# Kernel optimization log

Hardware: AMD Instinct MI355X
Metric: run time of the kernel (lower is better)

The kernel has to match this reference:

```python
import jax, jax.numpy as jnp
import numpy as np

NUM_HEADS = 16
QMAX = 127.0  # int8 symmetric

def fake_quant(x):
    # symmetric per-tensor int8 quantize -> dequantize (models Quantize/QLinear numerics)
    scale = jnp.maximum(jnp.max(jnp.abs(x)) / QMAX, 1e-8)
    q = jnp.clip(jnp.round(x / scale), -QMAX, QMAX) * scale
    # straight-through estimator (no-op in fwd-only, keeps fwd/bwd code identical)
    return x + jax.lax.stop_gradient(q - x)

def setup_inputs() -> dict:
    key = jax.random.key(0)
    ks = jax.random.split(key, 5)
    B, T, C = 2, 2048, 1024
    return {
        "x": jax.random.normal(ks[0], (B, T, C), jnp.float32),
        "Wqkv": jax.random.normal(ks[1], (3 * C, C), jnp.float32) * (C ** -0.5),
        "bqkv": jax.random.normal(ks[2], (3 * C,), jnp.float32) * 0.01,
        "Wproj": jax.random.normal(ks[3], (C, C), jnp.float32) * (C ** -0.5),
        "bproj": jax.random.normal(ks[4], (C,), jnp.float32) * 0.01,
    }

def reference(x, Wqkv, bqkv, Wproj, bproj):
    B, T, C = x.shape
    H = NUM_HEADS
    D = C // H
    scale = D ** -0.5
    # quantized input + quantized-weight linear (dequantized to fp32 afterwards)
    xq = fake_quant(x)
    qkv = xq @ fake_quant(Wqkv).T + bqkv                      # [B, T, 3C]
    qkv = qkv.reshape(B, T, 3, H, D).transpose(2, 0, 3, 1, 4)  # [3, B, H, T, D]
    q, k, v = qkv[0], qkv[1], qkv[2]
    scores = jnp.einsum("bhqd,bhkd->bhqk", q, k) * scale       # [B, H, T, T]
    causal = jnp.triu(jnp.full((T, T), -jnp.inf, jnp.float32), k=1)
    attn = jax.nn.softmax(scores + causal, axis=-1)
    # dropout: eval mode -> identity
    out = jnp.einsum("bhqk,bhkd->bhqd", attn, v)               # [B, H, T, D]
    out = out.transpose(0, 2, 1, 3).reshape(B, T, C)
    outq = fake_quant(out)
    return outq @ fake_quant(Wproj).T + bproj
```

## Files before the change

kernel.cpp:

```cpp
#include <hip/hip_runtime.h>
#include <hip/hip_bf16.h>
#include <stdint.h>

typedef __bf16 bf16_t;
typedef bf16_t bf16x4 __attribute__((ext_vector_type(4)));
typedef bf16_t bf16x8 __attribute__((ext_vector_type(8)));
typedef short s16x4 __attribute__((ext_vector_type(4)));
typedef int i32x4 __attribute__((ext_vector_type(4)));
typedef float f32x4 __attribute__((ext_vector_type(4)));
typedef unsigned int u32;
typedef u32 u32x4 __attribute__((ext_vector_type(4)));
typedef u32 u32x2 __attribute__((ext_vector_type(2)));

#define QMAXF 127.0f
#define CSC 0.18033688f

__device__ __forceinline__ void gl16(const void* g, void* l) {
  __builtin_amdgcn_global_load_lds(
      (__attribute__((address_space(1))) void*)(g),
      (__attribute__((address_space(3))) void*)(l), 16, 0, 0);
}

__global__ __launch_bounds__(256) void amax3_kernel(const float* __restrict__ p0, int n0,
                                                    const float* __restrict__ p1, int n1,
                                                    const float* __restrict__ p2, int n2,
                                                    float* __restrict__ dst) {
  const float* p; int n; float* d; int b0, nb;
  if (blockIdx.x < 512)      { p = p0; n = n0; d = dst + 0; b0 = 0;   nb = 512; }
  else if (blockIdx.x < 768) { p = p1; n = n1; d = dst + 1; b0 = 512; nb = 256; }
  else                       { p = p2; n = n2; d = dst + 2; b0 = 768; nb = 128; }
  const int n4 = n >> 2;
  const int stride = nb * 256;
  float m = 0.f;
  for (int i = (blockIdx.x - b0) * 256 + threadIdx.x; i < n4; i += stride) {
    const f32x4 v = ((const f32x4*)p)[i];
    m = fmaxf(m, fmaxf(fmaxf(fabsf(v[0]), fabsf(v[1])), fmaxf(fabsf(v[2]), fabsf(v[3]))));
  }
#pragma unroll
  for (int dd = 1; dd < 64; dd <<= 1) m = fmaxf(m, __shfl_xor(m, dd));
  __shared__ float sm[4];
  if ((threadIdx.x & 63) == 0) sm[threadIdx.x >> 6] = m;
  __syncthreads();
  if (threadIdx.x == 0) {
    float mm = fmaxf(fmaxf(sm[0], sm[1]), fmaxf(sm[2], sm[3]));
    atomicMax((int*)d, __float_as_int(mm));
  }
}

__device__ __forceinline__ void quant_body(const float* __restrict__ p, int n,
                                           const float* __restrict__ amax,
                                           int8_t* __restrict__ q, int bid, int nb) {
  const float s = fmaxf(amax[0] / QMAXF, 1e-8f);
  const int n4 = n >> 2;
  const int stride = nb * 256;
  for (int i = bid * 256 + (int)threadIdx.x; i < n4; i += stride) {
    const f32x4 v = ((const f32x4*)p)[i];
    int r[4];
#pragma unroll
    for (int j = 0; j < 4; j++) {
      float t = rintf(v[j] / s);
      t = fminf(127.f, fmaxf(-127.f, t));
      r[j] = (int)t;
    }
    ((uint32_t*)q)[i] = (uint32_t)(r[0] & 0xff) | ((uint32_t)(r[1] & 0xff) << 8) |
                        ((uint32_t)(r[2] & 0xff) << 16) | ((uint32_t)(r[3] & 0xff) << 24);
  }
}

__global__ __launch_bounds__(256) void quant3_kernel(const float* __restrict__ p0, int n0,
                                                     const float* __restrict__ p1, int n1,
                                                     const float* __restrict__ p2, int n2,
                                                     const float* __restrict__ amax,
                                                     int8_t* __restrict__ q0,
                                                     int8_t* __restrict__ q1,
                                                     int8_t* __restrict__ q2) {
  if (blockIdx.x < 512)      quant_body(p0, n0, amax + 0, q0, blockIdx.x, 512);
  else if (blockIdx.x < 768) quant_body(p1, n1, amax + 1, q1, blockIdx.x - 512, 256);
  else                       quant_body(p2, n2, amax + 2, q2, blockIdx.x - 768, 128);
}

__global__ __launch_bounds__(256) void quant_bf16_kernel(const u32* __restrict__ p,
                                                         int n,
                                                         const float* __restrict__ amax,
                                                         int8_t* __restrict__ q) {
  const float s = fmaxf(amax[0] / QMAXF, 1e-8f);
  const int n8 = n >> 3;
  const int stride = gridDim.x * blockDim.x;
  for (int i = blockIdx.x * blockDim.x + (int)threadIdx.x; i < n8; i += stride) {
    const u32x4 v = ((const u32x4*)p)[i];
    int r[8];
#pragma unroll
    for (int k = 0; k < 4; k++) {
      const float lo = __uint_as_float(v[k] << 16);
      const float hi = __uint_as_float(v[k] & 0xffff0000u);
      float t0 = fminf(127.f, fmaxf(-127.f, rintf(lo / s)));
      float t1 = fminf(127.f, fmaxf(-127.f, rintf(hi / s)));
      r[2 * k] = (int)t0; r[2 * k + 1] = (int)t1;
    }
    u32x2 o;
    o[0] = (u32)(r[0] & 0xff) | ((u32)(r[1] & 0xff) << 8) |
           ((u32)(r[2] & 0xff) << 16) | ((u32)(r[3] & 0xff) << 24);
    o[1] = (u32)(r[4] & 0xff) | ((u32)(r[5] & 0xff) << 8) |
           ((u32)(r[6] & 0xff) << 16) | ((u32)(r[7] & 0xff) << 24);
    ((u32x2*)q)[i] = o;
  }
}

template <int MODE>
__global__ __launch_bounds__(256) void gemm_i8_kernel(
    const int8_t* __restrict__ A, const int8_t* __restrict__ Bw,
    const float* __restrict__ amaxA, const float* __restrict__ amaxB,
    const float* __restrict__ bias,
    bf16_t* __restrict__ qkv_out, bf16_t* __restrict__ vt_out, float* __restrict__ f_out) {
  constexpr int K = 1024;
  __shared__ int8_t As[2][8192];
  __shared__ int8_t Bs[2][8192];
  const int tid = threadIdx.x;
  const int lane = tid & 63;
  const int w = tid >> 6, wr = w >> 1, wc = w & 1;
  const int l15 = lane & 15, lg = lane >> 4;
  const int bm = blockIdx.y * 128, bn = blockIdx.x * 128;

  const int sr = tid >> 2;
  const int sc = (tid & 3) * 16;
  const int8_t* gA = A + (size_t)(bm + sr) * K + sc;
  const int8_t* gB = Bw + (size_t)(bn + sr) * K + sc;

  auto stage = [&](int k0, int buf) {
    gl16(gA + k0, As[buf] + tid * 16);
    gl16(gA + 64 * K + k0, As[buf] + 4096 + tid * 16);
    gl16(gB + k0, Bs[buf] + tid * 16);
    gl16(gB + 64 * K + k0, Bs[buf] + 4096 + tid * 16);
  };

  i32x4 acc[4][4] = {};

  stage(0, 0);
  __syncthreads();
  for (int ks = 0; ks < K / 64; ks++) {
    const int buf = ks & 1;
    if (ks + 1 < K / 64) stage((ks + 1) * 64, buf ^ 1);
    i32x4 aF[4], bF[4];
#pragma unroll
    for (int m = 0; m < 4; m++)
      aF[m] = *(const i32x4*)(As[buf] + (wr * 64 + m * 16 + l15) * 64 + lg * 16);
#pragma unroll
    for (int n = 0; n < 4; n++)
      bF[n] = *(const i32x4*)(Bs[buf] + (wc * 64 + n * 16 + l15) * 64 + lg * 16);
#pragma unroll
    for (int m = 0; m < 4; m++)
#pragma unroll
      for (int n = 0; n < 4; n++)
        acc[m][n] = __builtin_amdgcn_mfma_i32_16x16x64_i8(aF[m], bF[n], acc[m][n], 0, 0, 0);
    __syncthreads();
  }

  const float sA = fmaxf(amaxA[0] / QMAXF, 1e-8f);
  const float sB = fmaxf(amaxB[0] / QMAXF, 1e-8f);
  const float s = sA * sB;

#pragma unroll
  for (int m = 0; m < 4; m++) {
#pragma unroll
    for (int n = 0; n < 4; n++) {
      const int c = bn + wc * 64 + n * 16 + l15;
      const float bs = bias[c];
      const int r0 = bm + wr * 64 + m * 16 + lg * 4;
      float vv[4];
#pragma unroll
      for (int reg = 0; reg < 4; reg++) vv[reg] = (float)acc[m][n][reg] * s + bs;
      if (MODE == 0) {
        const int which = c >> 10, hd = c & 1023;
        if (which < 2) {
          const float qs = (which == 0) ? CSC : 1.0f;
#pragma unroll
          for (int reg = 0; reg < 4; reg++) {
            const int r = r0 + reg;
            const int b = r >> 11, t = r & 2047;
            qkv_out[(size_t)which * (32u * 2048 * 64) +
                    (size_t)((((b << 4) + (hd >> 6)) * 2048 + t) << 6) + (hd & 63)] =
                (bf16_t)(vv[reg] * qs);
          }
        } else {
          const int b = r0 >> 11, t0 = r0 & 2047;
          const int h = hd >> 6, d = hd & 63;
          bf16x4 pk;
#pragma unroll
          for (int reg = 0; reg < 4; reg++) pk[reg] = (bf16_t)vv[reg];
          *(bf16x4*)(vt_out + ((size_t)((b << 4) + h) * 64 + d) * 2048 + t0) = pk;
        }
      } else {
#pragma unroll
        for (int reg = 0; reg < 4; reg++) f_out[(size_t)(r0 + reg) * 1024 + c] = vv[reg];
      }
    }
  }
}

__global__ __launch_bounds__(256, 2) void attn_kernel(
    const bf16_t* __restrict__ Qg, const bf16_t* __restrict__ Kg, const bf16_t* __restrict__ VTg,
    bf16_t* __restrict__ Out, float* __restrict__ amax_out) {
  const int bh = blockIdx.x;
  const int pairi = blockIdx.y;
  const int tid = threadIdx.x, lane = tid & 63, w = tid >> 6;
  const int l15 = lane & 15, lg = lane >> 4;
  const int b = bh >> 4, h = bh & 15;

  const bf16_t* Qp = Qg + (size_t)bh * 2048 * 64;
  const char* Kbase = (const char*)(Kg + (size_t)bh * 2048 * 64);
  const char* Vbase = (const char*)(VTg + (size_t)bh * 64 * 2048);

  __shared__ __align__(16) bf16_t Kb[3][4096];
  __shared__ __align__(16) bf16_t Vb[3][4096];

  auto stage = [&](int kv0, int buf) {
#pragma unroll
    for (int i = 0; i < 4; i++) {
      const int o = ((w & 1) * 4 + i) * 1024 + lane * 16;
      const int row = o >> 7;
      const int sbc = (o & 127) ^ ((row & 7) << 4);
      if (w < 2)
        gl16(Kbase + (size_t)(kv0 + row) * 128 + sbc, (char*)Kb[buf] + o);
      else
        gl16(Vbase + (size_t)row * 4096 + (size_t)kv0 * 2 + sbc, (char*)Vb[buf] + o);
    }
  };

  float am = 0.f;
  for (int half = 0; half < 2; ++half) {
    const int S = half ? (31 - pairi) : pairi;
    const int qb = S * 64 + w * 16;
    const int nt = S + 1;
    const int qrow = qb + l15;

    bf16x8 qf[2];
#pragma unroll
    for (int ks = 0; ks < 2; ks++)
      qf[ks] = *(const bf16x8*)(Qp + (size_t)(qb + l15) * 64 + ks * 32 + lg * 8);

    f32x4 acc[4] = {};
    float lsum = 0.f;

    stage(0, 0);
    if (nt > 1) stage(64, 1);

    for (int it = 0; it < nt; ++it) {
      const int sl = it % 3;
      const int kv0 = it * 64;

      if (it + 1 < nt) { asm volatile("s_waitcnt vmcnt(4)" ::: "memory"); }
      else             { asm volatile("s_waitcnt vmcnt(0)" ::: "memory"); }
      __builtin_amdgcn_sched_barrier(0);
      __builtin_amdgcn_s_barrier();
      __builtin_amdgcn_sched_barrier(0);

      if (it + 2 < nt) stage(kv0 + 128, (it + 2) % 3);

      bf16x8 kF[4][2];
#pragma unroll
      for (int rf = 0; rf < 4; rf++)
#pragma unroll
        for (int ks = 0; ks < 2; ks++) {
          const int row = rf * 16 + l15;
          kF[rf][ks] = *(const bf16x8*)((const char*)Kb[sl] + row * 128 +
                                        ((ks * 64 + lg * 16) ^ ((row & 7) << 4)));
        }
      s16x4 vB[4][4];
#pragma unroll
      for (int cf = 0; cf < 4; cf++)
#pragma unroll
        for (int rf = 0; rf < 4; rf++) {
          const int row = cf * 16 + l15;
          vB[cf][rf] = *(const s16x4*)((const char*)Vb[sl] + row * 128 +
                                       ((rf * 32 + lg * 8) ^ ((row & 7) << 4)));
        }

      f32x4 sfT[4] = {};
      __builtin_amdgcn_s_setprio(1);
#pragma unroll
      for (int rf = 0; rf < 4; rf++)
#pragma unroll
        for (int ks = 0; ks < 2; ks++)
          sfT[rf] = __builtin_amdgcn_mfma_f32_16x16x32_bf16(kF[rf][ks], qf[ks], sfT[rf], 0, 0, 0);
      __builtin_amdgcn_s_setprio(0);

      const bool need_mask = (it == nt - 1);
      float p[16];
#pragma unroll
      for (int rf = 0; rf < 4; rf++)
#pragma unroll
        for (int reg = 0; reg < 4; reg++) {
          float v = sfT[rf][reg];
          if (need_mask && (kv0 + rf * 16 + lg * 4 + reg > qrow)) v = -1e30f;
          p[rf * 4 + reg] = __builtin_amdgcn_exp2f(v);
        }
      float s01 = (p[0] + p[1]) + (p[2] + p[3]);
      float s23 = (p[4] + p[5]) + (p[6] + p[7]);
      float s45 = (p[8] + p[9]) + (p[10] + p[11]);
      float s67 = (p[12] + p[13]) + (p[14] + p[15]);
      lsum += (s01 + s23) + (s45 + s67);

      s16x4 pa[4];
#pragma unroll
      for (int rf = 0; rf < 4; rf++) {
        bf16x4 t;
#pragma unroll
        for (int reg = 0; reg < 4; reg++) t[reg] = (bf16_t)p[rf * 4 + reg];
        pa[rf] = __builtin_bit_cast(s16x4, t);
      }
      __builtin_amdgcn_s_setprio(1);
#pragma unroll
      for (int cf = 0; cf < 4; cf++)
#pragma unroll
        for (int rf = 0; rf < 4; rf++)
          acc[cf] = __builtin_amdgcn_mfma_f32_16x16x16bf16_1k(pa[rf], vB[cf][rf], acc[cf], 0, 0, 0);
      __builtin_amdgcn_s_setprio(0);
    }

    lsum += __shfl_xor(lsum, 16);
    lsum += __shfl_xor(lsum, 32);
    const float inv = 1.0f / lsum;
    float iq[4];
#pragma unroll
    for (int reg = 0; reg < 4; reg++) iq[reg] = __shfl(inv, lg * 4 + reg);
#pragma unroll
    for (int cf = 0; cf < 4; cf++)
#pragma unroll
      for (int reg = 0; reg < 4; reg++) {
        const float v = acc[cf][reg] * iq[reg];
        am = fmaxf(am, fabsf(v));
        const int t = qb + lg * 4 + reg;
        Out[(size_t)(b * 2048 + t) * 1024 + h * 64 + cf * 16 + l15] = (bf16_t)v;
      }

    __syncthreads();
  }

#pragma unroll
  for (int dd = 1; dd < 64; dd <<= 1) am = fmaxf(am, __shfl_xor(am, dd));
  if (lane == 0) atomicMax((int*)amax_out, __float_as_int(am));
}

extern "C" void kernel_launch(void* const* d_in, const int* in_sizes, int n_in,
                              void* d_out, int out_size, void* d_ws, size_t ws_size,
                              hipStream_t stream) {
  const float* x = (const float*)d_in[0];
  const float* Wqkv = (const float*)d_in[1];
  const float* bqkv = (const float*)d_in[2];
  const float* Wproj = (const float*)d_in[3];
  const float* bproj = (const float*)d_in[4];
  float* out = (float*)d_out;

  char* ws = (char*)d_ws;
  float* amax = (float*)ws;
  int8_t* xq = (int8_t*)(ws + 256);
  int8_t* wqq = xq + (size_t)4096 * 1024;
  int8_t* wpq = wqq + (size_t)3072 * 1024;
  bf16_t* qkv = (bf16_t*)(ws + 8388864);
  bf16_t* Q = qkv;
  bf16_t* Kk = qkv + (size_t)32 * 2048 * 64;
  bf16_t* VT = qkv + (size_t)2 * 32 * 2048 * 64;
  bf16_t* aout = (bf16_t*)(ws + 33554688);
  int8_t* outq = (int8_t*)(ws + 50331904);

  hipMemsetAsync(amax, 0, 16, stream);
  amax3_kernel<<<896, 256, 0, stream>>>(x, 4194304, Wqkv, 3145728, Wproj, 1048576, amax);
  quant3_kernel<<<896, 256, 0, stream>>>(x, 4194304, Wqkv, 3145728, Wproj, 1048576, amax,
                                         xq, wqq, wpq);
  gemm_i8_kernel<0><<<dim3(24, 32), 256, 0, stream>>>(xq, wqq, amax + 0, amax + 1, bqkv,
                                                      qkv, VT, nullptr);
  attn_kernel<<<dim3(32, 16), 256, 0, stream>>>(Q, Kk, VT, aout, amax + 3);
  quant_bf16_kernel<<<512, 256, 0, stream>>>((const u32*)aout, 4194304, amax + 3, outq);
  gemm_i8_kernel<1><<<dim3(8, 32), 256, 0, stream>>>(outq, wpq, amax + 3, amax + 2, bproj,
                                                     nullptr, nullptr, out);
}
```

Measured before the change: 129.7 us.

## Restructure attention into single-wave blocks loading K/V directly from global

```diff
diff --git a/kernel.cpp b/kernel.cpp
--- a/kernel.cpp
+++ b/kernel.cpp
@@ -197,144 +197,106 @@
   }
 }
 
-__global__ __launch_bounds__(256, 2) void attn_kernel(
+__global__ __launch_bounds__(64, 3) void attn_kernel(
     const bf16_t* __restrict__ Qg, const bf16_t* __restrict__ Kg, const bf16_t* __restrict__ VTg,
     bf16_t* __restrict__ Out, float* __restrict__ amax_out) {
   const int bh = blockIdx.x;
-  const int pairi = blockIdx.y;
-  const int tid = threadIdx.x, lane = tid & 63, w = tid >> 6;
+  const int S = 127 - (int)blockIdx.y;
+  const int lane = threadIdx.x;
   const int l15 = lane & 15, lg = lane >> 4;
   const int b = bh >> 4, h = bh & 15;
 
   const bf16_t* Qp = Qg + (size_t)bh * 2048 * 64;
-  const char* Kbase = (const char*)(Kg + (size_t)bh * 2048 * 64);
-  const char* Vbase = (const char*)(VTg + (size_t)bh * 64 * 2048);
-
-  __shared__ __align__(16) bf16_t Kb[3][4096];
-  __shared__ __align__(16) bf16_t Vb[3][4096];
-
-  auto stage = [&](int kv0, int buf) {
-#pragma unroll
-    for (int i = 0; i < 4; i++) {
-      const int o = ((w & 1) * 4 + i) * 1024 + lane * 16;
-      const int row = o >> 7;
-      const int sbc = (o & 127) ^ ((row & 7) << 4);
-      if (w < 2)
-        gl16(Kbase + (size_t)(kv0 + row) * 128 + sbc, (char*)Kb[buf] + o);
-      else
-        gl16(Vbase + (size_t)row * 4096 + (size_t)kv0 * 2 + sbc, (char*)Vb[buf] + o);
-    }
-  };
-
+  const bf16_t* Kp = Kg + (size_t)bh * 2048 * 64;
+  const bf16_t* Vp = VTg + (size_t)bh * 64 * 2048;
+
+  const int qb = S * 16;
+  const int nt = (S >> 2) + 1;
+  const int qrow = qb + l15;
+
+  bf16x8 qf[2];
+#pragma unroll
+  for (int ks = 0; ks < 2; ks++)
+    qf[ks] = *(const bf16x8*)(Qp + (size_t)(qb + l15) * 64 + ks * 32 + lg * 8);
+
+  f32x4 acc[4] = {};
+  float lsum = 0.f;
+
+  for (int it = 0; it < nt; ++it) {
+    const int kv0 = it * 64;
+
+    bf16x8 kF[4][2];
+#pragma unroll
+    for (int rf = 0; rf < 4; rf++)
+#pragma unroll
+      for (int ks = 0; ks < 2; ks++)
+        kF[rf][ks] = *(const bf16x8*)(Kp + (size_t)(kv0 + rf * 16 + l15) * 64 + ks * 32 + lg * 8);
+
+    s16x4 vB[4][4];
+#pragma unroll
+    for (int cf = 0; cf < 4; cf++)
+#pragma unroll
+      for (int rf = 0; rf < 4; rf++)
+        vB[cf][rf] = *(const s16x4*)(Vp + (size_t)(cf * 16 + l15) * 2048 + kv0 + rf * 16 + lg * 4);
+
+    f32x4 sfT[4] = {};
+    __builtin_amdgcn_s_setprio(1);
+#pragma unroll
+    for (int rf = 0; rf < 4; rf++)
+#pragma unroll
+      for (int ks = 0; ks < 2; ks++)
+        sfT[rf] = __builtin_amdgcn_mfma_f32_16x16x32_bf16(kF[rf][ks], qf[ks], sfT[rf], 0, 0, 0);
+    __builtin_amdgcn_s_setprio(0);
+
+    const bool need_mask = (it == nt - 1);
+    float p[16];
+#pragma unroll
+    for (int rf = 0; rf < 4; rf++)
+#pragma unroll
+      for (int reg = 0; reg < 4; reg++) {
+        float v = sfT[rf][reg];
+        if (need_mask && (kv0 + rf * 16 + lg * 4 + reg > qrow)) v = -1e30f;
+        p[rf * 4 + reg] = __builtin_amdgcn_exp2f(v);
+      }
+    float s01 = (p[0] + p[1]) + (p[2] + p[3]);
+    float s23 = (p[4] + p[5]) + (p[6] + p[7]);
+    float s45 = (p[8] + p[9]) + (p[10] + p[11]);
+    float s67 = (p[12] + p[13]) + (p[14] + p[15]);
+    lsum += (s01 + s23) + (s45 + s67);
+
+    s16x4 pa[4];
+#pragma unroll
+    for (int rf = 0; rf < 4; rf++) {
+      bf16x4 t;
+#pragma unroll
+      for (int reg = 0; reg < 4; reg++) t[reg] = (bf16_t)p[rf * 4 + reg];
+      pa[rf] = __builtin_bit_cast(s16x4, t);
+    }
+    __builtin_amdgcn_s_setprio(1);
+#pragma unroll
+    for (int cf = 0; cf < 4; cf++)
+#pragma unroll
+      for (int rf = 0; rf < 4; rf++)
+        acc[cf] = __builtin_amdgcn_mfma_f32_16x16x16bf16_1k(pa[rf], vB[cf][rf], acc[cf], 0, 0, 0);
+    __builtin_amdgcn_s_setprio(0);
+  }
+
+  lsum += __shfl_xor(lsum, 16);
+  lsum += __shfl_xor(lsum, 32);
+  const float inv = 1.0f / lsum;
+  float iq[4];
+#pragma unroll
+  for (int reg = 0; reg < 4; reg++) iq[reg] = __shfl(inv, lg * 4 + reg);
   float am = 0.f;
-  for (int half = 0; half < 2; ++half) {
-    const int S = half ? (31 - pairi) : pairi;
-    const int qb = S * 64 + w * 16;
-    const int nt = S + 1;
-    const int qrow = qb + l15;
-
-    bf16x8 qf[2];
-#pragma unroll
-    for (int ks = 0; ks < 2; ks++)
-      qf[ks] = *(const bf16x8*)(Qp + (size_t)(qb + l15) * 64 + ks * 32 + lg * 8);
-
-    f32x4 acc[4] = {};
-    float lsum = 0.f;
-
-    stage(0, 0);
-    if (nt > 1) stage(64, 1);
-
-    for (int it = 0; it < nt; ++it) {
-      const int sl = it % 3;
-      const int kv0 = it * 64;
-
-      if (it + 1 < nt) { asm volatile("s_waitcnt vmcnt(4)" ::: "memory"); }
-      else             { asm volatile("s_waitcnt vmcnt(0)" ::: "memory"); }
-      __builtin_amdgcn_sched_barrier(0);
-      __builtin_amdgcn_s_barrier();
-      __builtin_amdgcn_sched_barrier(0);
-
-      if (it + 2 < nt) stage(kv0 + 128, (it + 2) % 3);
-
-      bf16x8 kF[4][2];
-#pragma unroll
-      for (int rf = 0; rf < 4; rf++)
-#pragma unroll
-        for (int ks = 0; ks < 2; ks++) {
-          const int row = rf * 16 + l15;
-          kF[rf][ks] = *(const bf16x8*)((const char*)Kb[sl] + row * 128 +
-                                        ((ks * 64 + lg * 16) ^ ((row & 7) << 4)));
-        }
-      s16x4 vB[4][4];
-#pragma unroll
-      for (int cf = 0; cf < 4; cf++)
-#pragma unroll
-        for (int rf = 0; rf < 4; rf++) {
-          const int row = cf * 16 + l15;
-          vB[cf][rf] = *(const s16x4*)((const char*)Vb[sl] + row * 128 +
-                                       ((rf * 32 + lg * 8) ^ ((row & 7) << 4)));
-        }
-
-      f32x4 sfT[4] = {};
-      __builtin_amdgcn_s_setprio(1);
-#pragma unroll
-      for (int rf = 0; rf < 4; rf++)
-#pragma unroll
-        for (int ks = 0; ks < 2; ks++)
-          sfT[rf] = __builtin_amdgcn_mfma_f32_16x16x32_bf16(kF[rf][ks], qf[ks], sfT[rf], 0, 0, 0);
-      __builtin_amdgcn_s_setprio(0);
-
-      const bool need_mask = (it == nt - 1);
-      float p[16];
-#pragma unroll
-      for (int rf = 0; rf < 4; rf++)
-#pragma unroll
-        for (int reg = 0; reg < 4; reg++) {
-          float v = sfT[rf][reg];
-          if (need_mask && (kv0 + rf * 16 + lg * 4 + reg > qrow)) v = -1e30f;
-          p[rf * 4 + reg] = __builtin_amdgcn_exp2f(v);
-        }
-      float s01 = (p[0] + p[1]) + (p[2] + p[3]);
-      float s23 = (p[4] + p[5]) + (p[6] + p[7]);
-      float s45 = (p[8] + p[9]) + (p[10] + p[11]);
-      float s67 = (p[12] + p[13]) + (p[14] + p[15]);
-      lsum += (s01 + s23) + (s45 + s67);
-
-      s16x4 pa[4];
-#pragma unroll
-      for (int rf = 0; rf < 4; rf++) {
-        bf16x4 t;
-#pragma unroll
-        for (int reg = 0; reg < 4; reg++) t[reg] = (bf16_t)p[rf * 4 + reg];
-        pa[rf] = __builtin_bit_cast(s16x4, t);
-      }
-      __builtin_amdgcn_s_setprio(1);
-#pragma unroll
-      for (int cf = 0; cf < 4; cf++)
-#pragma unroll
-        for (int rf = 0; rf < 4; rf++)
-          acc[cf] = __builtin_amdgcn_mfma_f32_16x16x16bf16_1k(pa[rf], vB[cf][rf], acc[cf], 0, 0, 0);
-      __builtin_amdgcn_s_setprio(0);
-    }
-
-    lsum += __shfl_xor(lsum, 16);
-    lsum += __shfl_xor(lsum, 32);
-    const float inv = 1.0f / lsum;
-    float iq[4];
-#pragma unroll
-    for (int reg = 0; reg < 4; reg++) iq[reg] = __shfl(inv, lg * 4 + reg);
-#pragma unroll
-    for (int cf = 0; cf < 4; cf++)
-#pragma unroll
-      for (int reg = 0; reg < 4; reg++) {
-        const float v = acc[cf][reg] * iq[reg];
-        am = fmaxf(am, fabsf(v));
-        const int t = qb + lg * 4 + reg;
-        Out[(size_t)(b * 2048 + t) * 1024 + h * 64 + cf * 16 + l15] = (bf16_t)v;
-      }
-
-    __syncthreads();
-  }
+#pragma unroll
+  for (int cf = 0; cf < 4; cf++)
+#pragma unroll
+    for (int reg = 0; reg < 4; reg++) {
+      const float v = acc[cf][reg] * iq[reg];
+      am = fmaxf(am, fabsf(v));
+      const int t = qb + lg * 4 + reg;
+      Out[(size_t)(b * 2048 + t) * 1024 + h * 64 + cf * 16 + l15] = (bf16_t)v;
+    }
 
 #pragma unroll
   for (int dd = 1; dd < 64; dd <<= 1) am = fmaxf(am, __shfl_xor(am, dd));
@@ -369,7 +331,7 @@
                                          xq, wqq, wpq);
   gemm_i8_kernel<0><<<dim3(24, 32), 256, 0, stream>>>(xq, wqq, amax + 0, amax + 1, bqkv,
                                                       qkv, VT, nullptr);
-  attn_kernel<<<dim3(32, 16), 256, 0, stream>>>(Q, Kk, VT, aout, amax + 3);
+  attn_kernel<<<dim3(32, 128), 64, 0, stream>>>(Q, Kk, VT, aout, amax + 3);
   quant_bf16_kernel<<<512, 256, 0, stream>>>((const u32*)aout, 4194304, amax + 3, outq);
   gemm_i8_kernel<1><<<dim3(8, 32), 256, 0, stream>>>(outq, wpq, amax + 3, amax + 2, bproj,
                                                      nullptr, nullptr, out);
```

Result: slower. 258.2 us, median of 2 (+99.1%).

## Load V directly from global in attention and split projection GEMM with smaller M tile

Applied to the files above, without the earlier changes.

```diff
diff --git a/kernel.cpp b/kernel.cpp
--- a/kernel.cpp
+++ b/kernel.cpp
@@ -106,12 +106,11 @@
   }
 }
 
-template <int MODE>
-__global__ __launch_bounds__(256) void gemm_i8_kernel(
+__global__ __launch_bounds__(256) void gemm_qkv_kernel(
     const int8_t* __restrict__ A, const int8_t* __restrict__ Bw,
     const float* __restrict__ amaxA, const float* __restrict__ amaxB,
     const float* __restrict__ bias,
-    bf16_t* __restrict__ qkv_out, bf16_t* __restrict__ vt_out, float* __restrict__ f_out) {
+    bf16_t* __restrict__ qkv_out, bf16_t* __restrict__ vt_out) {
   constexpr int K = 1024;
   __shared__ int8_t As[2][8192];
   __shared__ int8_t Bs[2][8192];
@@ -169,30 +168,89 @@
       float vv[4];
 #pragma unroll
       for (int reg = 0; reg < 4; reg++) vv[reg] = (float)acc[m][n][reg] * s + bs;
-      if (MODE == 0) {
-        const int which = c >> 10, hd = c & 1023;
-        if (which < 2) {
-          const float qs = (which == 0) ? CSC : 1.0f;
-#pragma unroll
-          for (int reg = 0; reg < 4; reg++) {
-            const int r = r0 + reg;
-            const int b = r >> 11, t = r & 2047;
-            qkv_out[(size_t)which * (32u * 2048 * 64) +
-                    (size_t)((((b << 4) + (hd >> 6)) * 2048 + t) << 6) + (hd & 63)] =
-                (bf16_t)(vv[reg] * qs);
-          }
-        } else {
-          const int b = r0 >> 11, t0 = r0 & 2047;
-          const int h = hd >> 6, d = hd & 63;
-          bf16x4 pk;
-#pragma unroll
-          for (int reg = 0; reg < 4; reg++) pk[reg] = (bf16_t)vv[reg];
-          *(bf16x4*)(vt_out + ((size_t)((b << 4) + h) * 64 + d) * 2048 + t0) = pk;
+      const int which = c >> 10, hd = c & 1023;
+      if (which < 2) {
+        const float qs = (which == 0) ? CSC : 1.0f;
+#pragma unroll
+        for (int reg = 0; reg < 4; reg++) {
+          const int r = r0 + reg;
+          const int b = r >> 11, t = r & 2047;
+          qkv_out[(size_t)which * (32u * 2048 * 64) +
+                  (size_t)((((b << 4) + (hd >> 6)) * 2048 + t) << 6) + (hd & 63)] =
+              (bf16_t)(vv[reg] * qs);
         }
       } else {
-#pragma unroll
-        for (int reg = 0; reg < 4; reg++) f_out[(size_t)(r0 + reg) * 1024 + c] = vv[reg];
+        const int b = r0 >> 11, t0 = r0 & 2047;
+        const int h = hd >> 6, d = hd & 63;
+        bf16x4 pk;
+#pragma unroll
+        for (int reg = 0; reg < 4; reg++) pk[reg] = (bf16_t)vv[reg];
+        *(bf16x4*)(vt_out + ((size_t)((b << 4) + h) * 64 + d) * 2048 + t0) = pk;
       }
+    }
+  }
+}
+
+__global__ __launch_bounds__(256) void gemm_proj_kernel(
+    const int8_t* __restrict__ A, const int8_t* __restrict__ Bw,
+    const float* __restrict__ amaxA, const float* __restrict__ amaxB,
+    const float* __restrict__ bias, float* __restrict__ f_out) {
+  constexpr int K = 1024;
+  __shared__ int8_t As[2][4096];
+  __shared__ int8_t Bs[2][8192];
+  const int tid = threadIdx.x;
+  const int lane = tid & 63;
+  const int w = tid >> 6, wr = w >> 1, wc = w & 1;
+  const int l15 = lane & 15, lg = lane >> 4;
+  const int bm = blockIdx.y * 64, bn = blockIdx.x * 128;
+
+  const int sr = tid >> 2;
+  const int sc = (tid & 3) * 16;
+  const int8_t* gA = A + (size_t)(bm + sr) * K + sc;
+  const int8_t* gB = Bw + (size_t)(bn + sr) * K + sc;
+
+  auto stage = [&](int k0, int buf) {
+    gl16(gA + k0, As[buf] + tid * 16);
+    gl16(gB + k0, Bs[buf] + tid * 16);
+    gl16(gB + 64 * K + k0, Bs[buf] + 4096 + tid * 16);
+  };
+
+  i32x4 acc[2][4] = {};
+
+  stage(0, 0);
+  __syncthreads();
+  for (int ks = 0; ks < K / 64; ks++) {
+    const int buf = ks & 1;
+    if (ks + 1 < K / 64) stage((ks + 1) * 64, buf ^ 1);
+    i32x4 aF[2], bF[4];
+#pragma unroll
+    for (int m = 0; m < 2; m++)
+      aF[m] = *(const i32x4*)(As[buf] + (wr * 32 + m * 16 + l15) * 64 + lg * 16);
+#pragma unroll
+    for (int n = 0; n < 4; n++)
+      bF[n] = *(const i32x4*)(Bs[buf] + (wc * 64 + n * 16 + l15) * 64 + lg * 16);
+#pragma unroll
+    for (int m = 0; m < 2; m++)
+#pragma unroll
+      for (int n = 0; n < 4; n++)
+        acc[m][n] = __builtin_amdgcn_mfma_i32_16x16x64_i8(aF[m], bF[n], acc[m][n], 0, 0, 0);
+    __syncthreads();
+  }
+
+  const float sA = fmaxf(amaxA[0] / QMAXF, 1e-8f);
+  const float sB = fmaxf(amaxB[0] / QMAXF, 1e-8f);
+  const float s = sA * sB;
+
+#pragma unroll
+  for (int m = 0; m < 2; m++) {
+#pragma unroll
+    for (int n = 0; n < 4; n++) {
+      const int c = bn + wc * 64 + n * 16 + l15;
+      const float bs = bias[c];
+      const int r0 = bm + wr * 32 + m * 16 + lg * 4;
+#pragma unroll
+      for (int reg = 0; reg < 4; reg++)
+        f_out[(size_t)(r0 + reg) * 1024 + c] = (float)acc[m][n][reg] * s + bs;
     }
   }
 }
@@ -208,21 +266,17 @@
 
   const bf16_t* Qp = Qg + (size_t)bh * 2048 * 64;
   const char* Kbase = (const char*)(Kg + (size_t)bh * 2048 * 64);
-  const char* Vbase = (const char*)(VTg + (size_t)bh * 64 * 2048);
+  const bf16_t* Vp = VTg + (size_t)bh * 64 * 2048;
 
   __shared__ __align__(16) bf16_t Kb[3][4096];
-  __shared__ __align__(16) bf16_t Vb[3][4096];
-
-  auto stage = [&](int kv0, int buf) {
-#pragma unroll
-    for (int i = 0; i < 4; i++) {
-      const int o = ((w & 1) * 4 + i) * 1024 + lane * 16;
+
+  auto stageK = [&](int kv0, int buf) {
+#pragma unroll
+    for (int i = 0; i < 2; i++) {
+      const int o = (w * 2 + i) * 1024 + lane * 16;
       const int row = o >> 7;
       const int sbc = (o & 127) ^ ((row & 7) << 4);
-      if (w < 2)
-        gl16(Kbase + (size_t)(kv0 + row) * 128 + sbc, (char*)Kb[buf] + o);
-      else
-        gl16(Vbase + (size_t)row * 4096 + (size_t)kv0 * 2 + sbc, (char*)Vb[buf] + o);
+      gl16(Kbase + (size_t)(kv0 + row) * 128 + sbc, (char*)Kb[buf] + o);
     }
   };
 
@@ -241,20 +295,28 @@
     f32x4 acc[4] = {};
     float lsum = 0.f;
 
-    stage(0, 0);
-    if (nt > 1) stage(64, 1);
+    stageK(0, 0);
+    if (nt > 1) stageK(64, 1);
 
     for (int it = 0; it < nt; ++it) {
       const int sl = it % 3;
       const int kv0 = it * 64;
 
-      if (it + 1 < nt) { asm volatile("s_waitcnt vmcnt(4)" ::: "memory"); }
+      if (it + 1 < nt) { asm volatile("s_waitcnt vmcnt(2)" ::: "memory"); }
       else             { asm volatile("s_waitcnt vmcnt(0)" ::: "memory"); }
       __builtin_amdgcn_sched_barrier(0);
       __builtin_amdgcn_s_barrier();
       __builtin_amdgcn_sched_barrier(0);
 
-      if (it + 2 < nt) stage(kv0 + 128, (it + 2) % 3);
+      s16x4 vB[4][4];
+      {
+        const bf16_t* vb = Vp + kv0 + lg * 4;
+#pragma unroll
+        for (int cf = 0; cf < 4; cf++)
+#pragma unroll
+          for (int rf = 0; rf < 4; rf++)
+            vB[cf][rf] = *(const s16x4*)(vb + (size_t)(cf * 16 + l15) * 2048 + rf * 16);
+      }
 
       bf16x8 kF[4][2];
 #pragma unroll
@@ -265,15 +327,9 @@
           kF[rf][ks] = *(const bf16x8*)((const char*)Kb[sl] + row * 128 +
                                         ((ks * 64 + lg * 16) ^ ((row & 7) << 4)));
         }
-      s16x4 vB[4][4];
-#pragma unroll
-      for (int cf = 0; cf < 4; cf++)
-#pragma unroll
-        for (int rf = 0; rf < 4; rf++) {
-          const int row = cf * 16 + l15;
-          vB[cf][rf] = *(const s16x4*)((const char*)Vb[sl] + row * 128 +
-                                       ((rf * 32 + lg * 8) ^ ((row & 7) << 4)));
-        }
+      if (it + 2 < nt) stageK(kv0 + 128, (it + 2) % 3);
+      asm volatile("s_waitcnt lgkmcnt(0)" ::: "memory");
+      __builtin_amdgcn_sched_barrier(0);
 
       f32x4 sfT[4] = {};
       __builtin_amdgcn_s_setprio(1);
@@ -367,10 +423,9 @@
   amax3_kernel<<<896, 256, 0, stream>>>(x, 4194304, Wqkv, 3145728, Wproj, 1048576, amax);
   quant3_kernel<<<896, 256, 0, stream>>>(x, 4194304, Wqkv, 3145728, Wproj, 1048576, amax,
                                          xq, wqq, wpq);
-  gemm_i8_kernel<0><<<dim3(24, 32), 256, 0, stream>>>(xq, wqq, amax + 0, amax + 1, bqkv,
-                                                      qkv, VT, nullptr);
+  gemm_qkv_kernel<<<dim3(24, 32), 256, 0, stream>>>(xq, wqq, amax + 0, amax + 1, bqkv,
+                                                    qkv, VT);
   attn_kernel<<<dim3(32, 16), 256, 0, stream>>>(Q, Kk, VT, aout, amax + 3);
   quant_bf16_kernel<<<512, 256, 0, stream>>>((const u32*)aout, 4194304, amax + 3, outq);
-  gemm_i8_kernel<1><<<dim3(8, 32), 256, 0, stream>>>(outq, wpq, amax + 3, amax + 2, bproj,
-                                                     nullptr, nullptr, out);
-}
+  gemm_proj_kernel<<<dim3(8, 64), 256, 0, stream>>>(outq, wpq, amax + 3, amax + 2, bproj, out);
+}
```

After: 215.4 us. 1.66x slower.
